# Kernel optimization log

Measured on AMD Instinct MI355X. Metric: run time of the kernel, lower is better.

Reference implementation:

```python
import jax, jax.numpy as jnp
import numpy as np
from jax import lax

DIM = 64


def _dwconv(x, w, b):
    # x: [B,C,H,W], w: [C,1,kh,kw] depthwise, 'same' padding
    kh, kw = w.shape[2], w.shape[3]
    y = lax.conv_general_dilated(
        x, w, window_strides=(1, 1),
        padding=[(kh // 2, kh // 2), (kw // 2, kw // 2)],
        dimension_numbers=("NCHW", "OIHW", "NCHW"),
        feature_group_count=x.shape[1])
    return y + b[None, :, None, None]


def _conv1x1(x, w, b):
    y = lax.conv_general_dilated(
        x, w, window_strides=(1, 1), padding="VALID",
        dimension_numbers=("NCHW", "OIHW", "NCHW"))
    return y + b[None, :, None, None]


def _avgpool3(x):
    # PyTorch AvgPool2d(3,1,1) default count_include_pad=True -> sum/9
    s = lax.reduce_window(x, 0.0, lax.add, (1, 1, 3, 3), (1, 1, 1, 1),
                          [(0, 0), (0, 0), (1, 1), (1, 1)])
    return s / 9.0


def _maxpool3(x):
    return lax.reduce_window(x, -jnp.inf, lax.max, (1, 1, 3, 3), (1, 1, 1, 1),
                             [(0, 0), (0, 0), (1, 1), (1, 1)])


def setup_inputs() -> dict:
    key = jax.random.key(0)
    ks = jax.random.split(key, 18)
    C = DIM
    def w(k, shape):
        fan_in = shape[1] * shape[2] * shape[3]
        bound = 1.0 / np.sqrt(fan_in)
        return jax.random.uniform(k, shape, jnp.float32, -bound, bound)
    def b(k, fan_in):
        bound = 1.0 / np.sqrt(fan_in)
        return jax.random.uniform(k, (C,), jnp.float32, -bound, bound)
    return {
        "x": jax.random.normal(ks[0], (16, C, 128, 128), jnp.float32),
        "w55": w(ks[1], (C, 1, 5, 5)), "b55": b(ks[2], 25),
        "w17_0": w(ks[3], (C, 1, 1, 7)), "b17_0": b(ks[4], 7),
        "w17_1": w(ks[5], (C, 1, 7, 1)), "b17_1": b(ks[6], 7),
        "w111_0": w(ks[7], (C, 1, 1, 11)), "b111_0": b(ks[8], 11),
        "w111_1": w(ks[9], (C, 1, 11, 1)), "b111_1": b(ks[10], 11),
        "w211_0": w(ks[11], (C, 1, 1, 21)), "b211_0": b(ks[12], 21),
        "w211_1": w(ks[13], (C, 1, 21, 1)), "b211_1": b(ks[14], 21),
        "w11": w(ks[15], (C, C, 1, 1)), "b11": b(ks[16], C),
    }


def reference(x, w55, b55, w17_0, b17_0, w17_1, b17_1,
              w111_0, b111_0, w111_1, b111_1,
              w211_0, b211_0, w211_1, b211_1, w11, b11):
    def branch(inp):
        c55 = _dwconv(inp, w55, b55)
        c17 = _dwconv(_dwconv(inp, w17_0, b17_0), w17_1, b17_1)
        c111 = _dwconv(_dwconv(inp, w111_0, b111_0), w111_1, b111_1)
        c211 = _dwconv(_dwconv(inp, w211_0, b211_0), w211_1, b211_1)
        return _conv1x1(c55 + c17 + c111 + c211, w11, b11)

    mixer = branch(x)
    mixer_1 = branch(_avgpool3(x))
    mixer_2 = branch(_maxpool3(x))
    return (mixer + mixer_1 + mixer_2) * x
```

## Files before the change

### kernel.cpp

```cpp
#include <hip/hip_runtime.h>
#include <hip/hip_bf16.h>
#include <cstdint>

#define HH 128
#define WW 128
#define CC 64
#define BB 16
#define PLANE (HH*WW)
#define TPSTR 16512

#define XS_STR    52
#define XRAW_STR  60
#define XSTH_H    8736
#define H7_H      11328
#define UNION_F   7072
#define H11_H     14144
#define H21_H     16960
#define SMEM_FLOATS 12232

__device__ __forceinline__ float lo16(unsigned int u) {
  return __uint_as_float(u << 16);
}
__device__ __forceinline__ float hi16(unsigned int u) {
  return __uint_as_float(u & 0xffff0000u);
}

__global__ __launch_bounds__(256, 3) void k_dwsum(
    const float* __restrict__ x, float* __restrict__ T,
    const float* __restrict__ w55, const float* __restrict__ b55,
    const float* __restrict__ w17_0, const float* __restrict__ b17_0,
    const float* __restrict__ w17_1, const float* __restrict__ b17_1,
    const float* __restrict__ w111_0, const float* __restrict__ b111_0,
    const float* __restrict__ w111_1, const float* __restrict__ b111_1,
    const float* __restrict__ w211_0, const float* __restrict__ b211_0,
    const float* __restrict__ w211_1, const float* __restrict__ b211_1) {
  __shared__ float sm[SMEM_FLOATS];
  __hip_bfloat16* hb = (__hip_bfloat16*)sm;

  const int bid = blockIdx.x;
  const int pl = bid >> 3;
  const int t = bid & 7;
  const int tR0 = (t >> 2) * 64;
  const int tC0 = (t & 3) * 32;
  const int ch = pl & (CC - 1);
  const float* xp = x + (size_t)pl * PLANE;
  float* Tp = T + (size_t)pl * TPSTR;
  const int tid = threadIdx.x;

  {
    float* xraw = sm + UNION_F;
    const int base_r = tR0 - 11, base_c = tC0 - 12;
    for (int i = tid; i < 86 * 14; i += 256) {
      int rr = i / 14;
      int jj = i - rr * 14;
      int gr = base_r + rr;
      int gc = base_c + jj * 4;
      float4 v = make_float4(0.f, 0.f, 0.f, 0.f);
      if ((unsigned)gr < 128u && (unsigned)gc < 128u)
        v = *(const float4*)(xp + gr * WW + gc);
      *(float4*)(xraw + rr * XRAW_STR + jj * 4) = v;
    }
  }
  __syncthreads();

  {
    const float* xraw = sm + UNION_F;
    __hip_bfloat16* xsTh = hb + XSTH_H;
    for (int i = tid; i < 28 * 13; i += 256) {
      int rg = i % 28;
      int jj = i / 28;
      int rr0 = rg * 3;
      const float* rp = xraw + rr0 * XRAW_STR + jj * 4;
      float w[5][8];
      #pragma unroll
      for (int k = 0; k < 5; ++k) {
        float4 a = *(const float4*)(rp + k * XRAW_STR);
        float4 b = *(const float4*)(rp + k * XRAW_STR + 4);
        w[k][0] = a.x; w[k][1] = a.y; w[k][2] = a.z; w[k][3] = a.w;
        w[k][4] = b.x; w[k][5] = b.y; w[k][6] = b.z; w[k][7] = b.w;
      }
      int gc0 = tC0 + jj * 4 - 12;
      bool cv[7];
      #pragma unroll
      for (int p = 1; p <= 6; ++p) cv[p] = (unsigned)(gc0 + p) < 128u;

      #pragma unroll
      for (int k = 0; k < 3; ++k) {
        int rr = rr0 + k;
        int gr = tR0 + rr - 10;
        bool rv0 = (unsigned)(gr - 1) < 128u;
        bool rv1 = (unsigned)(gr) < 128u;
        bool rv2 = (unsigned)(gr + 1) < 128u;
        float M0[7], M1[7], M2[7];
        #pragma unroll
        for (int p = 1; p <= 6; ++p) {
          M0[p] = (rv0 && cv[p]) ? w[k][p] : -3.402823466e38f;
          M1[p] = (rv1 && cv[p]) ? w[k + 1][p] : -3.402823466e38f;
          M2[p] = (rv2 && cv[p]) ? w[k + 2][p] : -3.402823466e38f;
        }
        float uq[4];
        #pragma unroll
        for (int q = 0; q < 4; ++q) {
          float s = w[k][q + 1] + w[k][q + 2] + w[k][q + 3] + w[k + 1][q + 1] +
                    w[k + 1][q + 2] + w[k + 1][q + 3] + w[k + 2][q + 1] +
                    w[k + 2][q + 2] + w[k + 2][q + 3];
          float m = fmaxf(
              fmaxf(fmaxf(M0[q + 1], M0[q + 2]), fmaxf(M0[q + 3], M1[q + 1])),
              fmaxf(fmaxf(M1[q + 2], M1[q + 3]),
                    fmaxf(fmaxf(M2[q + 1], M2[q + 2]), M2[q + 3])));
          float val = w[k + 1][q + 2] + s * (1.f / 9.f) + m;
          bool vo = rv1 && ((unsigned)(gc0 + q + 2) < 128u);
          uq[q] = vo ? val : 0.f;
        }
        *(float4*)(sm + rr * XS_STR + jj * 4) =
            make_float4(uq[0], uq[1], uq[2], uq[3]);
        int rt = rr - 8;
        if ((unsigned)rt < 68u) {
          #pragma unroll
          for (int q = 0; q < 4; ++q) {
            int ct = jj * 4 + q - 8;
            if ((unsigned)ct < 36u)
              xsTh[ct * 72 + rt] = __float2bfloat16(uq[q]);
          }
        }
      }
    }
  }

  float k7[7], k11[11], k21[21];
  #pragma unroll
  for (int i = 0; i < 7; ++i) k7[i] = w17_0[ch * 7 + i];
  #pragma unroll
  for (int i = 0; i < 11; ++i) k11[i] = w111_0[ch * 11 + i];
  #pragma unroll
  for (int i = 0; i < 21; ++i) k21[i] = w211_0[ch * 21 + i];
  float bb7 = 3.f * b17_0[ch];
  float bb11 = 3.f * b111_0[ch];
  float bb21 = 3.f * b211_0[ch];

  __syncthreads();

  for (int it = tid; it < 84 * 4; it += 256) {
    int rr = it % 84;
    int cg = it / 84;
    float w[28];
    const float* xr = sm + rr * XS_STR + cg * 8;
    #pragma unroll
    for (int j = 0; j < 7; ++j) {
      float4 v = *(const float4*)(xr + 4 * j);
      w[4 * j] = v.x; w[4 * j + 1] = v.y; w[4 * j + 2] = v.z; w[4 * j + 3] = v.w;
    }
    int gr = tR0 + rr - 10;
    bool rv = (unsigned)gr < 128u;
    bool v11r = (rr >= 5) && (rr <= 78);
    bool v7r = (rr >= 7) && (rr <= 76);
    #pragma unroll
    for (int j = 0; j < 8; ++j) {
      float a21 = bb21, a11 = bb11, a7 = bb7;
      #pragma unroll
      for (int d = 0; d < 21; ++d) a21 += k21[d] * w[j + d];
      #pragma unroll
      for (int d = 0; d < 11; ++d) a11 += k11[d] * w[j + 5 + d];
      #pragma unroll
      for (int d = 0; d < 7; ++d) a7 += k7[d] * w[j + 7 + d];
      int c = cg * 8 + j;
      hb[H21_H + c * 88 + rr] = __float2bfloat16(rv ? a21 : 0.f);
      if (v11r) hb[H11_H + c * 88 + rr - 5] = __float2bfloat16(rv ? a11 : 0.f);
      if (v7r) hb[H7_H + c * 88 + rr - 7] = __float2bfloat16(rv ? a7 : 0.f);
    }
  }

  float v7a[7], v11a[11], v21a[21], w5a[25];
  #pragma unroll
  for (int i = 0; i < 7; ++i) v7a[i] = w17_1[ch * 7 + i];
  #pragma unroll
  for (int i = 0; i < 11; ++i) v11a[i] = w111_1[ch * 11 + i];
  #pragma unroll
  for (int i = 0; i < 21; ++i) v21a[i] = w211_1[ch * 21 + i];
  #pragma unroll
  for (int i = 0; i < 25; ++i) w5a[i] = w55[ch * 25 + i];
  float bsum = 3.f * (b55[ch] + b17_1[ch] + b111_1[ch] + b211_1[ch]);

  __syncthreads();

  {
    int c = tid & 31;
    int r0 = (tid >> 5) * 8;
    float acc[8];
    #pragma unroll
    for (int j = 0; j < 8; ++j) acc[j] = bsum;

    float A[28];
    {
      const unsigned* p = (const unsigned*)&hb[H21_H + c * 88 + r0];
      uint4 q0 = *(const uint4*)p;
      uint4 q1 = *(const uint4*)(p + 4);
      uint4 q2 = *(const uint4*)(p + 8);
      uint2 q3 = *(const uint2*)(p + 12);
      A[0]=lo16(q0.x);A[1]=hi16(q0.x);A[2]=lo16(q0.y);A[3]=hi16(q0.y);
      A[4]=lo16(q0.z);A[5]=hi16(q0.z);A[6]=lo16(q0.w);A[7]=hi16(q0.w);
      A[8]=lo16(q1.x);A[9]=hi16(q1.x);A[10]=lo16(q1.y);A[11]=hi16(q1.y);
      A[12]=lo16(q1.z);A[13]=hi16(q1.z);A[14]=lo16(q1.w);A[15]=hi16(q1.w);
      A[16]=lo16(q2.x);A[17]=hi16(q2.x);A[18]=lo16(q2.y);A[19]=hi16(q2.y);
      A[20]=lo16(q2.z);A[21]=hi16(q2.z);A[22]=lo16(q2.w);A[23]=hi16(q2.w);
      A[24]=lo16(q3.x);A[25]=hi16(q3.x);A[26]=lo16(q3.y);A[27]=hi16(q3.y);
      #pragma unroll
      for (int d = 0; d < 21; ++d)
        #pragma unroll
        for (int j = 0; j < 8; ++j) acc[j] += v21a[d] * A[d + j];
    }
    {
      const unsigned* p = (const unsigned*)&hb[H11_H + c * 88 + r0];
      uint4 q0 = *(const uint4*)p;
      uint4 q1 = *(const uint4*)(p + 4);
      uint2 q2 = *(const uint2*)(p + 8);
      A[0]=lo16(q0.x);A[1]=hi16(q0.x);A[2]=lo16(q0.y);A[3]=hi16(q0.y);
      A[4]=lo16(q0.z);A[5]=hi16(q0.z);A[6]=lo16(q0.w);A[7]=hi16(q0.w);
      A[8]=lo16(q1.x);A[9]=hi16(q1.x);A[10]=lo16(q1.y);A[11]=hi16(q1.y);
      A[12]=lo16(q1.z);A[13]=hi16(q1.z);A[14]=lo16(q1.w);A[15]=hi16(q1.w);
      A[16]=lo16(q2.x);A[17]=hi16(q2.x);
      #pragma unroll
      for (int d = 0; d < 11; ++d)
        #pragma unroll
        for (int j = 0; j < 8; ++j) acc[j] += v11a[d] * A[d + j];
    }
    {
      const unsigned* p = (const unsigned*)&hb[H7_H + c * 88 + r0];
      uint4 q0 = *(const uint4*)p;
      uint4 q1 = *(const uint4*)(p + 4);
      A[0]=lo16(q0.x);A[1]=hi16(q0.x);A[2]=lo16(q0.y);A[3]=hi16(q0.y);
      A[4]=lo16(q0.z);A[5]=hi16(q0.z);A[6]=lo16(q0.w);A[7]=hi16(q0.w);
      A[8]=lo16(q1.x);A[9]=hi16(q1.x);A[10]=lo16(q1.y);A[11]=hi16(q1.y);
      A[12]=lo16(q1.z);A[13]=hi16(q1.z);
      #pragma unroll
      for (int d = 0; d < 7; ++d)
        #pragma unroll
        for (int j = 0; j < 8; ++j) acc[j] += v7a[d] * A[d + j];
    }
    {
      #pragma unroll
      for (int dc = 0; dc < 5; ++dc) {
        const unsigned* p = (const unsigned*)&hb[XSTH_H + (c + dc) * 72 + r0];
        uint4 q0 = *(const uint4*)p;
        uint2 q1 = *(const uint2*)(p + 4);
        float X[12];
        X[0]=lo16(q0.x);X[1]=hi16(q0.x);X[2]=lo16(q0.y);X[3]=hi16(q0.y);
        X[4]=lo16(q0.z);X[5]=hi16(q0.z);X[6]=lo16(q0.w);X[7]=hi16(q0.w);
        X[8]=lo16(q1.x);X[9]=hi16(q1.x);X[10]=lo16(q1.y);X[11]=hi16(q1.y);
        #pragma unroll
        for (int dr = 0; dr < 5; ++dr)
          #pragma unroll
          for (int j = 0; j < 8; ++j) acc[j] += w5a[dr * 5 + dc] * X[j + dr];
      }
    }
    #pragma unroll
    for (int j = 0; j < 8; ++j)
      Tp[(size_t)(tR0 + r0 + j) * WW + tC0 + c] = acc[j];
  }
}

__global__ __launch_bounds__(256) void k_mix(const float* __restrict__ T,
                                             const float* __restrict__ x,
                                             const float* __restrict__ w11,
                                             const float* __restrict__ b11,
                                             float* __restrict__ out) {
  __shared__ float Wt[64 * 68];
  int bid = blockIdx.x;
  int b = bid >> 7;
  int px0 = (bid & 127) * 128;
  int tid = threadIdx.x;

  for (int i = tid; i < 4096; i += 256) {
    int co = i >> 6, ci = i & 63;
    Wt[ci * 68 + co] = w11[i];
  }
  __syncthreads();

  int pxg = tid & 31;
  int cog = tid >> 5;
  const float* Tb = T + (size_t)b * 64 * TPSTR + px0 + pxg * 4;
  const float* wp = Wt + cog * 8;

  float acc[8][4];
  #pragma unroll
  for (int a = 0; a < 8; ++a)
    #pragma unroll
    for (int p = 0; p < 4; ++p) acc[a][p] = 0.f;

  float4 tb[3][4];
  #pragma unroll
  for (int kk = 0; kk < 4; ++kk)
    tb[0][kk] = *(const float4*)(Tb + (size_t)kk * TPSTR);
  #pragma unroll
  for (int kk = 0; kk < 4; ++kk)
    tb[1][kk] = *(const float4*)(Tb + (size_t)(4 + kk) * TPSTR);

  #pragma unroll
  for (int kc = 0; kc < 16; ++kc) {
    const int cur = kc % 3;
    if (kc < 14) {
      const int nxt = (kc + 2) % 3;
      #pragma unroll
      for (int kk = 0; kk < 4; ++kk)
        tb[nxt][kk] =
            *(const float4*)(Tb + (size_t)((kc + 2) * 4 + kk) * TPSTR);
    }
    #pragma unroll
    for (int kk = 0; kk < 4; ++kk) {
      int k = kc * 4 + kk;
      float4 q0 = *(const float4*)(wp + k * 68);
      float4 q1 = *(const float4*)(wp + k * 68 + 4);
      float wf[8] = {q0.x, q0.y, q0.z, q0.w, q1.x, q1.y, q1.z, q1.w};
      float4 tv = tb[cur][kk];
      float tvv[4] = {tv.x, tv.y, tv.z, tv.w};
      #pragma unroll
      for (int a = 0; a < 8; ++a)
        #pragma unroll
        for (int p = 0; p < 4; ++p) acc[a][p] += wf[a] * tvv[p];
    }
  }

  const float* xb = x + (size_t)b * (CC * PLANE) + px0 + pxg * 4;
  float* ob = out + (size_t)b * (CC * PLANE) + px0 + pxg * 4;
  #pragma unroll
  for (int a = 0; a < 8; ++a) {
    int co = cog * 8 + a;
    float bb = 3.f * b11[co];
    float4 xv = *(const float4*)(xb + (size_t)co * PLANE);
    float4 o;
    o.x = (acc[a][0] + bb) * xv.x;
    o.y = (acc[a][1] + bb) * xv.y;
    o.z = (acc[a][2] + bb) * xv.z;
    o.w = (acc[a][3] + bb) * xv.w;
    *(float4*)(ob + (size_t)co * PLANE) = o;
  }
}

extern "C" void kernel_launch(void* const* d_in, const int* in_sizes, int n_in,
                              void* d_out, int out_size, void* d_ws,
                              size_t ws_size, hipStream_t stream) {
  const float* x = (const float*)d_in[0];
  const float* w55 = (const float*)d_in[1];
  const float* b55 = (const float*)d_in[2];
  const float* w17_0 = (const float*)d_in[3];
  const float* b17_0 = (const float*)d_in[4];
  const float* w17_1 = (const float*)d_in[5];
  const float* b17_1 = (const float*)d_in[6];
  const float* w111_0 = (const float*)d_in[7];
  const float* b111_0 = (const float*)d_in[8];
  const float* w111_1 = (const float*)d_in[9];
  const float* b111_1 = (const float*)d_in[10];
  const float* w211_0 = (const float*)d_in[11];
  const float* b211_0 = (const float*)d_in[12];
  const float* w211_1 = (const float*)d_in[13];
  const float* b211_1 = (const float*)d_in[14];
  const float* w11 = (const float*)d_in[15];
  const float* b11 = (const float*)d_in[16];
  float* outp = (float*)d_out;

  float* T = (float*)d_ws;

  k_dwsum<<<BB * CC * 8, 256, 0, stream>>>(
      x, T, w55, b55, w17_0, b17_0, w17_1, b17_1, w111_0, b111_0, w111_1,
      b111_1, w211_0, b211_0, w211_1, b211_1);
  k_mix<<<BB * 128, 256, 0, stream>>>(T, x, w11, b11, outp);
}
```

Measured before the change: 300.5 us.

## Halve raw-input staging buffer and store intermediate in row-major channel layout

The raw-input staging and pool/max preprocessing phase now runs in two halves, each loading 44 rows into a smaller shared buffer. This cuts shared memory per block so the launch bound can rise from 3 to 4 blocks per CU. The intermediate T tensor also moves from per-channel planes to a [batch][row][channel][col] layout, so the 1x1 mixing kernel reads all 64 channels of a row from one contiguous 32KB region instead of 64 strided planes. The cost is extra barriers and a second load pass.

```diff
diff --git a/kernel.cpp b/kernel.cpp
--- a/kernel.cpp
+++ b/kernel.cpp
@@ -7,7 +7,8 @@
 #define CC 64
 #define BB 16
 #define PLANE (HH*WW)
-#define TPSTR 16512
+#define TROW   8192
+#define TBATCH (128*TROW)
 
 #define XS_STR    52
 #define XRAW_STR  60
@@ -16,7 +17,7 @@
 #define UNION_F   7072
 #define H11_H     14144
 #define H21_H     16960
-#define SMEM_FLOATS 12232
+#define SMEM_FLOATS 9888
 
 __device__ __forceinline__ float lo16(unsigned int u) {
   return __uint_as_float(u << 16);
@@ -25,7 +26,72 @@
   return __uint_as_float(u & 0xffff0000u);
 }
 
-__global__ __launch_bounds__(256, 3) void k_dwsum(
+__device__ __forceinline__ void phase_a2_half(
+    float* sm, __hip_bfloat16* hb, const float* xbuf, int tid, int tR0,
+    int tC0, int rg_lo, int roff) {
+  __hip_bfloat16* xsTh = hb + XSTH_H;
+  for (int i = tid; i < 14 * 13; i += 256) {
+    int rg = rg_lo + (i % 14);
+    int jj = i / 14;
+    int rr0 = rg * 3;
+    const float* rp = xbuf + (rr0 - roff) * XRAW_STR + jj * 4;
+    float w[5][8];
+    #pragma unroll
+    for (int k = 0; k < 5; ++k) {
+      float4 a = *(const float4*)(rp + k * XRAW_STR);
+      float4 b = *(const float4*)(rp + k * XRAW_STR + 4);
+      w[k][0] = a.x; w[k][1] = a.y; w[k][2] = a.z; w[k][3] = a.w;
+      w[k][4] = b.x; w[k][5] = b.y; w[k][6] = b.z; w[k][7] = b.w;
+    }
+    int gc0 = tC0 + jj * 4 - 12;
+    bool cv[7];
+    #pragma unroll
+    for (int p = 1; p <= 6; ++p) cv[p] = (unsigned)(gc0 + p) < 128u;
+
+    #pragma unroll
+    for (int k = 0; k < 3; ++k) {
+      int rr = rr0 + k;
+      int gr = tR0 + rr - 10;
+      bool rv0 = (unsigned)(gr - 1) < 128u;
+      bool rv1 = (unsigned)(gr) < 128u;
+      bool rv2 = (unsigned)(gr + 1) < 128u;
+      float M0[7], M1[7], M2[7];
+      #pragma unroll
+      for (int p = 1; p <= 6; ++p) {
+        M0[p] = (rv0 && cv[p]) ? w[k][p] : -3.402823466e38f;
+        M1[p] = (rv1 && cv[p]) ? w[k + 1][p] : -3.402823466e38f;
+        M2[p] = (rv2 && cv[p]) ? w[k + 2][p] : -3.402823466e38f;
+      }
+      float uq[4];
+      #pragma unroll
+      for (int q = 0; q < 4; ++q) {
+        float s = w[k][q + 1] + w[k][q + 2] + w[k][q + 3] + w[k + 1][q + 1] +
+                  w[k + 1][q + 2] + w[k + 1][q + 3] + w[k + 2][q + 1] +
+                  w[k + 2][q + 2] + w[k + 2][q + 3];
+        float m = fmaxf(
+            fmaxf(fmaxf(M0[q + 1], M0[q + 2]), fmaxf(M0[q + 3], M1[q + 1])),
+            fmaxf(fmaxf(M1[q + 2], M1[q + 3]),
+                  fmaxf(fmaxf(M2[q + 1], M2[q + 2]), M2[q + 3])));
+        float val = w[k + 1][q + 2] + s * (1.f / 9.f) + m;
+        bool vo = rv1 && ((unsigned)(gc0 + q + 2) < 128u);
+        uq[q] = vo ? val : 0.f;
+      }
+      *(float4*)(sm + rr * XS_STR + jj * 4) =
+          make_float4(uq[0], uq[1], uq[2], uq[3]);
+      int rt = rr - 8;
+      if ((unsigned)rt < 68u) {
+        #pragma unroll
+        for (int q = 0; q < 4; ++q) {
+          int ct = jj * 4 + q - 8;
+          if ((unsigned)ct < 36u)
+            xsTh[ct * 72 + rt] = __float2bfloat16(uq[q]);
+        }
+      }
+    }
+  }
+}
+
+__global__ __launch_bounds__(256, 4) void k_dwsum(
     const float* __restrict__ x, float* __restrict__ T,
     const float* __restrict__ w55, const float* __restrict__ b55,
     const float* __restrict__ w17_0, const float* __restrict__ b17_0,
@@ -43,89 +109,39 @@
   const int tR0 = (t >> 2) * 64;
   const int tC0 = (t & 3) * 32;
   const int ch = pl & (CC - 1);
+  const int bb2 = pl >> 6;
   const float* xp = x + (size_t)pl * PLANE;
-  float* Tp = T + (size_t)pl * TPSTR;
+  float* Tp = T + (size_t)bb2 * TBATCH + (size_t)ch * 128;
   const int tid = threadIdx.x;
 
-  {
-    float* xraw = sm + UNION_F;
-    const int base_r = tR0 - 11, base_c = tC0 - 12;
-    for (int i = tid; i < 86 * 14; i += 256) {
-      int rr = i / 14;
-      int jj = i - rr * 14;
-      int gr = base_r + rr;
-      int gc = base_c + jj * 4;
-      float4 v = make_float4(0.f, 0.f, 0.f, 0.f);
-      if ((unsigned)gr < 128u && (unsigned)gc < 128u)
-        v = *(const float4*)(xp + gr * WW + gc);
-      *(float4*)(xraw + rr * XRAW_STR + jj * 4) = v;
-    }
-  }
-  __syncthreads();
-
-  {
-    const float* xraw = sm + UNION_F;
-    __hip_bfloat16* xsTh = hb + XSTH_H;
-    for (int i = tid; i < 28 * 13; i += 256) {
-      int rg = i % 28;
-      int jj = i / 28;
-      int rr0 = rg * 3;
-      const float* rp = xraw + rr0 * XRAW_STR + jj * 4;
-      float w[5][8];
-      #pragma unroll
-      for (int k = 0; k < 5; ++k) {
-        float4 a = *(const float4*)(rp + k * XRAW_STR);
-        float4 b = *(const float4*)(rp + k * XRAW_STR + 4);
-        w[k][0] = a.x; w[k][1] = a.y; w[k][2] = a.z; w[k][3] = a.w;
-        w[k][4] = b.x; w[k][5] = b.y; w[k][6] = b.z; w[k][7] = b.w;
-      }
-      int gc0 = tC0 + jj * 4 - 12;
-      bool cv[7];
-      #pragma unroll
-      for (int p = 1; p <= 6; ++p) cv[p] = (unsigned)(gc0 + p) < 128u;
-
-      #pragma unroll
-      for (int k = 0; k < 3; ++k) {
-        int rr = rr0 + k;
-        int gr = tR0 + rr - 10;
-        bool rv0 = (unsigned)(gr - 1) < 128u;
-        bool rv1 = (unsigned)(gr) < 128u;
-        bool rv2 = (unsigned)(gr + 1) < 128u;
-        float M0[7], M1[7], M2[7];
-        #pragma unroll
-        for (int p = 1; p <= 6; ++p) {
-          M0[p] = (rv0 && cv[p]) ? w[k][p] : -3.402823466e38f;
-          M1[p] = (rv1 && cv[p]) ? w[k + 1][p] : -3.402823466e38f;
-          M2[p] = (rv2 && cv[p]) ? w[k + 2][p] : -3.402823466e38f;
-        }
-        float uq[4];
-        #pragma unroll
-        for (int q = 0; q < 4; ++q) {
-          float s = w[k][q + 1] + w[k][q + 2] + w[k][q + 3] + w[k + 1][q + 1] +
-                    w[k + 1][q + 2] + w[k + 1][q + 3] + w[k + 2][q + 1] +
-                    w[k + 2][q + 2] + w[k + 2][q + 3];
-          float m = fmaxf(
-              fmaxf(fmaxf(M0[q + 1], M0[q + 2]), fmaxf(M0[q + 3], M1[q + 1])),
-              fmaxf(fmaxf(M1[q + 2], M1[q + 3]),
-                    fmaxf(fmaxf(M2[q + 1], M2[q + 2]), M2[q + 3])));
-          float val = w[k + 1][q + 2] + s * (1.f / 9.f) + m;
-          bool vo = rv1 && ((unsigned)(gc0 + q + 2) < 128u);
-          uq[q] = vo ? val : 0.f;
-        }
-        *(float4*)(sm + rr * XS_STR + jj * 4) =
-            make_float4(uq[0], uq[1], uq[2], uq[3]);
-        int rt = rr - 8;
-        if ((unsigned)rt < 68u) {
-          #pragma unroll
-          for (int q = 0; q < 4; ++q) {
-            int ct = jj * 4 + q - 8;
-            if ((unsigned)ct < 36u)
-              xsTh[ct * 72 + rt] = __float2bfloat16(uq[q]);
-          }
-        }
-      }
-    }
-  }
+  float* xbuf = sm + UNION_F;
+  const int base_r = tR0 - 11, base_c = tC0 - 12;
+
+  for (int i = tid; i < 44 * 14; i += 256) {
+    int rr = i / 14;
+    int jj = i - rr * 14;
+    int gr = base_r + rr;
+    int gc = base_c + jj * 4;
+    float4 v = make_float4(0.f, 0.f, 0.f, 0.f);
+    if ((unsigned)gr < 128u && (unsigned)gc < 128u)
+      v = *(const float4*)(xp + gr * WW + gc);
+    *(float4*)(xbuf + rr * XRAW_STR + jj * 4) = v;
+  }
+  __syncthreads();
+  phase_a2_half(sm, hb, xbuf, tid, tR0, tC0, 0, 0);
+  __syncthreads();
+  for (int i = tid; i < 44 * 14; i += 256) {
+    int rr = i / 14;
+    int jj = i - rr * 14;
+    int gr = base_r + 42 + rr;
+    int gc = base_c + jj * 4;
+    float4 v = make_float4(0.f, 0.f, 0.f, 0.f);
+    if ((unsigned)gr < 128u && (unsigned)gc < 128u)
+      v = *(const float4*)(xp + gr * WW + gc);
+    *(float4*)(xbuf + rr * XRAW_STR + jj * 4) = v;
+  }
+  __syncthreads();
+  phase_a2_half(sm, hb, xbuf, tid, tR0, tC0, 14, 42);
 
   float k7[7], k11[11], k21[21];
   #pragma unroll
@@ -255,7 +271,7 @@
     }
     #pragma unroll
     for (int j = 0; j < 8; ++j)
-      Tp[(size_t)(tR0 + r0 + j) * WW + tC0 + c] = acc[j];
+      Tp[(size_t)(tR0 + r0 + j) * TROW + tC0 + c] = acc[j];
   }
 }
 
@@ -267,7 +283,8 @@
   __shared__ float Wt[64 * 68];
   int bid = blockIdx.x;
   int b = bid >> 7;
-  int px0 = (bid & 127) * 128;
+  int row = bid & 127;
+  int px0 = row * 128;
   int tid = threadIdx.x;
 
   for (int i = tid; i < 4096; i += 256) {
@@ -278,7 +295,7 @@
 
   int pxg = tid & 31;
   int cog = tid >> 5;
-  const float* Tb = T + (size_t)b * 64 * TPSTR + px0 + pxg * 4;
+  const float* Tb = T + (size_t)b * TBATCH + (size_t)row * TROW + pxg * 4;
   const float* wp = Wt + cog * 8;
 
   float acc[8][4];
@@ -290,10 +307,10 @@
   float4 tb[3][4];
   #pragma unroll
   for (int kk = 0; kk < 4; ++kk)
-    tb[0][kk] = *(const float4*)(Tb + (size_t)kk * TPSTR);
+    tb[0][kk] = *(const float4*)(Tb + (size_t)kk * 128);
   #pragma unroll
   for (int kk = 0; kk < 4; ++kk)
-    tb[1][kk] = *(const float4*)(Tb + (size_t)(4 + kk) * TPSTR);
+    tb[1][kk] = *(const float4*)(Tb + (size_t)(4 + kk) * 128);
 
   #pragma unroll
   for (int kc = 0; kc < 16; ++kc) {
@@ -303,7 +320,7 @@
       #pragma unroll
       for (int kk = 0; kk < 4; ++kk)
         tb[nxt][kk] =
-            *(const float4*)(Tb + (size_t)((kc + 2) * 4 + kk) * TPSTR);
+            *(const float4*)(Tb + (size_t)((kc + 2) * 4 + kk) * 128);
     }
     #pragma unroll
     for (int kk = 0; kk < 4; ++kk) {
```

Measured after the change: 283.0 us. 5.8% less time.
